# Optimization experiments

Measured on AMD Instinct MI355X. Metric: run time of the kernel, lower is better.

Reference implementation:

```python
import jax, jax.numpy as jnp
import numpy as np

D = 512      # embedding_dimension
L1 = 1024    # english sentence length
L2 = 1024    # french sentence length
V1 = 32000   # english vocab
V2 = 32000   # french vocab
NNEG = 8192  # negative samples
SCALE = 0.05 # param init scale (keeps exp() stable)


def setup_inputs() -> dict:
    key = jax.random.key(0)
    ks = jax.random.split(key, 32)
    def n(k, shape):
        return jax.random.normal(k, shape, dtype=jnp.float32) * SCALE
    inp = {}
    inp["en"] = jax.random.randint(ks[0], (L1,), 0, V1)
    inp["fr"] = jax.random.randint(ks[1], (L2,), 0, V2)
    inp["en_neg"] = jax.random.randint(ks[2], (NNEG,), 0, V1)
    inp["fr_neg"] = jax.random.randint(ks[3], (NNEG,), 0, V2)
    # input embeddings
    inp["emb"] = n(ks[4], (V1, D))
    # 3-layer BiLSTM, hidden=D per direction; layer0 in=D, layers 1-2 in=2D
    inp["Wih0"] = n(ks[5], (2, 4 * D, D)); inp["Whh0"] = n(ks[6], (2, 4 * D, D)); inp["b0"] = n(ks[7], (2, 4 * D))
    inp["Wih1"] = n(ks[8], (2, 4 * D, 2 * D)); inp["Whh1"] = n(ks[9], (2, 4 * D, D)); inp["b1"] = n(ks[10], (2, 4 * D))
    inp["Wih2"] = n(ks[11], (2, 4 * D, 2 * D)); inp["Whh2"] = n(ks[12], (2, 4 * D, D)); inp["b2"] = n(ks[13], (2, 4 * D))
    # inference nets (mu and sigma, 2-layer each)
    inp["Wmu1"] = n(ks[14], (D, D)); inp["bmu1"] = n(ks[15], (D,))
    inp["Wmu2"] = n(ks[16], (D, D)); inp["bmu2"] = n(ks[17], (D,))
    inp["Ws1"] = n(ks[18], (D, D)); inp["bs1"] = n(ks[19], (D,))
    inp["Ws2"] = n(ks[20], (D, D)); inp["bs2"] = n(ks[21], (D,))
    # softmax-approximation embedding tables
    inp["E_en"] = n(ks[22], (V1, D))
    inp["E_fr"] = n(ks[23], (V2, D))
    # reparameterization noise (epsilon.sample() per token, made explicit)
    inp["eps"] = jax.random.normal(ks[24], (L1, D), dtype=jnp.float32)
    return inp


def _lstm_bidir(xs, Wih, Whh, b):
    # xs: (L, in); Wih: (2, 4D, in); Whh: (2, 4D, D); b: (2, 4D)
    def run(d, reverse):
        Wi, Wh, bb = Wih[d], Whh[d], b[d]
        def step(carry, x):
            h, c = carry
            g = Wi @ x + Wh @ h + bb
            i, f, gg, o = jnp.split(g, 4)
            i = jax.nn.sigmoid(i); f = jax.nn.sigmoid(f)
            gg = jnp.tanh(gg); o = jax.nn.sigmoid(o)
            c = f * c + i * gg
            h = o * jnp.tanh(c)
            return (h, c), h
        init = (jnp.zeros((Wh.shape[1],), xs.dtype), jnp.zeros((Wh.shape[1],), xs.dtype))
        _, hs = jax.lax.scan(step, init, xs, reverse=reverse)
        return hs
    return run(0, False), run(1, True)  # each (L, D)


def reference(en, fr, en_neg, fr_neg, emb,
              Wih0, Whh0, b0, Wih1, Whh1, b1, Wih2, Whh2, b2,
              Wmu1, bmu1, Wmu2, bmu2, Ws1, bs1, Ws2, bs2,
              E_en, E_fr, eps):
    x = emb[en]                                   # (L1, D)
    hf, hb = _lstm_bidir(x, Wih0, Whh0, b0)
    hf, hb = _lstm_bidir(jnp.concatenate([hf, hb], -1), Wih1, Whh1, b1)
    hf, hb = _lstm_bidir(jnp.concatenate([hf, hb], -1), Wih2, Whh2, b2)
    h = hf + hb                                   # fwd+bwd hidden sum (intermediate[0][0]+intermediate[0][1])
    mu = jax.nn.relu(h @ Wmu1.T + bmu1) @ Wmu2.T + bmu2
    sigma = jax.nn.softplus(jax.nn.relu(h @ Ws1.T + bs1) @ Ws2.T + bs2)
    z = mu + eps * sigma                          # reparameterized sample (L1, D)
    # closed-form KL( N(mu, diag(sigma^2)) || N(0, I) ), summed over tokens
    kl = 0.5 * jnp.sum(sigma ** 2 + mu ** 2 - 1.0 - 2.0 * jnp.log(sigma))
    # english negative-sampling softmax approximation, summed over tokens
    pos = jnp.exp(jnp.sum(z * E_en[en], axis=-1))            # (L1,)
    neg = jnp.sum(jnp.exp(z @ E_en[en_neg].T), axis=-1)      # (L1,)
    sum_x = jnp.sum(pos / (pos + neg))
    # alignment scoring: every french token vs every english latent z
    s = jnp.exp(z @ E_fr[fr].T)                               # (L1, L2)
    negf = jnp.sum(jnp.exp(z @ E_fr[fr_neg].T), -1, keepdims=True)  # (L1, 1)
    p = s / (s + negf)                                        # (L1, L2)
    sum_y = jnp.sum(p) / L1                                   # uniform-alignment marginal
    return -(sum_x + sum_y - kl)


if __name__ == "__main__":
    out = reference(**setup_inputs())
    print(out)
```

## Files before the change

### kernel.cpp

```cpp
#include <hip/hip_runtime.h>
#include <hip/hip_bf16.h>


template<bool GATHER, bool RELU, int EPI>
__global__ __launch_bounds__(256) void gemm_nt(
    const float* __restrict__ A, const float* __restrict__ B,
    const float* __restrict__ bias, const int* __restrict__ idx,
    float* __restrict__ C, const float* __restrict__ negf,
    float* __restrict__ outsum, int M, int N, int K)
{
    __shared__ float As[16][68];
    __shared__ float Bs[16][68];
    __shared__ float wsum[4];

    const int tid = threadIdx.x;
    const int bm = blockIdx.x, bn = blockIdx.y;
    const int tx = tid & 15, ty = tid >> 4;
    const int lr = tid >> 2;
    const int lk = (tid & 3) * 4;

    const long arow = (long)bm * 64 + lr;
    const int  brow = bn * 64 + lr;
    const long bsrc = GATHER ? (long)idx[brow] : (long)brow;
    const float* Ap = A + arow * K + lk;
    const float* Bp = B + bsrc * K + lk;

    float acc[4][4] = {};

    for (int k0 = 0; k0 < K; k0 += 16) {
        float4 av = *(const float4*)(Ap + k0);
        float4 bv = *(const float4*)(Bp + k0);
        __syncthreads();
        As[lk + 0][lr] = av.x; As[lk + 1][lr] = av.y;
        As[lk + 2][lr] = av.z; As[lk + 3][lr] = av.w;
        Bs[lk + 0][lr] = bv.x; Bs[lk + 1][lr] = bv.y;
        Bs[lk + 2][lr] = bv.z; Bs[lk + 3][lr] = bv.w;
        __syncthreads();
#pragma unroll
        for (int k = 0; k < 16; ++k) {
            float4 a = *(const float4*)&As[k][ty * 4];
            float4 b = *(const float4*)&Bs[k][tx * 4];
            float ar[4] = {a.x, a.y, a.z, a.w};
            float br[4] = {b.x, b.y, b.z, b.w};
#pragma unroll
            for (int i = 0; i < 4; ++i)
#pragma unroll
                for (int j = 0; j < 4; ++j)
                    acc[i][j] += ar[i] * br[j];
        }
    }

    const int row0 = bm * 64 + ty * 4, col0 = bn * 64 + tx * 4;

    if (EPI == 0) {
#pragma unroll
        for (int i = 0; i < 4; ++i) {
            float4 v;
            float vv[4];
#pragma unroll
            for (int j = 0; j < 4; ++j) {
                float x = acc[i][j];
                if (bias) x += bias[col0 + j];
                if (RELU) x = x > 0.f ? x : 0.f;
                vv[j] = x;
            }
            v.x = vv[0]; v.y = vv[1]; v.z = vv[2]; v.w = vv[3];
            *(float4*)&C[(long)(row0 + i) * N + col0] = v;
        }
    } else if (EPI == 1) {
#pragma unroll
        for (int i = 0; i < 4; ++i) {
            float s = expf(acc[i][0]) + expf(acc[i][1]) +
                      expf(acc[i][2]) + expf(acc[i][3]);
            s += __shfl_xor(s, 1); s += __shfl_xor(s, 2);
            s += __shfl_xor(s, 4); s += __shfl_xor(s, 8);
            if (tx == 0) atomicAdd(&C[row0 + i], s);
        }
    } else {
        float t = 0.f;
#pragma unroll
        for (int i = 0; i < 4; ++i) {
            float nf = negf[row0 + i];
#pragma unroll
            for (int j = 0; j < 4; ++j) {
                float e = expf(acc[i][j]);
                t += e / (e + nf);
            }
        }
#pragma unroll
        for (int o = 1; o < 64; o <<= 1) t += __shfl_xor(t, o);
        if ((tid & 63) == 0) wsum[tid >> 6] = t;
        __syncthreads();
        if (tid == 0) atomicAdd(outsum, wsum[0] + wsum[1] + wsum[2] + wsum[3]);
    }
}

__global__ __launch_bounds__(256, 1) void lstm_scan(
    const float* __restrict__ Xf, const float* __restrict__ Xb,
    const float* __restrict__ Whh,
    float* __restrict__ out,
    unsigned long long* __restrict__ hbuf)
{
    const int tid  = threadIdx.x;
    const int dir  = blockIdx.x >> 7;
    const int w    = blockIdx.x & 127;
    const int r    = tid >> 4;
    const int ck   = tid & 15;
    const int gate = r >> 2;
    const int jl   = r & 3;
    const int j    = w * 4 + jl;
    const int grow = gate * 512 + j;

    __shared__ float Wl[256 * 36];
    __shared__ float hs[16 * 36];
    __shared__ float ga[16];

    {
        const float4* Wrow = (const float4*)(Whh + ((long)dir * 2048 + grow) * 512 + ck * 32);
        float4* wl4 = (float4*)Wl + tid * 9;
#pragma unroll
        for (int q = 0; q < 8; ++q) wl4[q] = Wrow[q];
    }
    __syncthreads();

    const float* Xp = dir ? Xb : Xf;
    unsigned long long* myh = hbuf + dir * 1024;

    float c = 0.f;
    bool dead = false;

    const float4* wl4 = (const float4*)Wl + tid * 9;
    const float4* hs4 = (const float4*)hs + ck * 9;

    for (int s = 0; s < 1024; ++s) {
        const int t = dir ? (1023 - s) : s;
        float xg = Xp[(long)t * 2048 + grow];

        unsigned long long* rb = myh + ((s + 1) & 1) * 512;
        unsigned long long v0, v1;
        unsigned it = 0;
        for (;;) {
            v0 = __hip_atomic_load(&rb[tid],       __ATOMIC_RELAXED, __HIP_MEMORY_SCOPE_AGENT);
            v1 = __hip_atomic_load(&rb[tid + 256], __ATOMIC_RELAXED, __HIP_MEMORY_SCOPE_AGENT);
            if (dead || ((int)(v0 >> 32) == s && (int)(v1 >> 32) == s)) break;
            if (++it > (1u << 20)) { dead = true; break; }
        }
        hs[((tid) >> 5) * 36 + (tid & 31)]             = __uint_as_float((unsigned)v0);
        hs[((tid + 256) >> 5) * 36 + (tid & 31)]       = __uint_as_float((unsigned)v1);
        __syncthreads();

        float a0 = 0.f, a1 = 0.f;
#pragma unroll
        for (int q = 0; q < 8; q += 2) {
            float4 w0 = wl4[q],     h0 = hs4[q];
            float4 w1 = wl4[q + 1], h1 = hs4[q + 1];
            a0 += w0.x*h0.x + w0.y*h0.y + w0.z*h0.z + w0.w*h0.w;
            a1 += w1.x*h1.x + w1.y*h1.y + w1.z*h1.z + w1.w*h1.w;
        }
        float acc = a0 + a1;
        acc += __shfl_xor(acc, 1);
        acc += __shfl_xor(acc, 2);
        acc += __shfl_xor(acc, 4);
        acc += __shfl_xor(acc, 8);
        if (ck == 0) ga[r] = acc + xg;
        __syncthreads();

        if (tid < 4) {
            float gi = ga[tid], gf = ga[4 + tid], gg = ga[8 + tid], go = ga[12 + tid];
            float i_ = 1.f / (1.f + __expf(-gi));
            float f_ = 1.f / (1.f + __expf(-gf));
            float eg = __expf(2.f * gg);
            float g_ = (eg - 1.f) / (eg + 1.f);
            float o_ = 1.f / (1.f + __expf(-go));
            c = f_ * c + i_ * g_;
            float ec = __expf(2.f * c);
            float tc = (ec - 1.f) / (ec + 1.f);
            float h = o_ * tc;
            unsigned long long pk = (unsigned long long)__float_as_uint(h)
                                  | ((unsigned long long)(unsigned)(s + 1) << 32);
            __hip_atomic_store(&myh[(s & 1) * 512 + w * 4 + tid], pk,
                               __ATOMIC_RELAXED, __HIP_MEMORY_SCOPE_AGENT);
            out[(long)t * 1024 + dir * 512 + w * 4 + tid] = h;
        }
    }
}

__global__ __launch_bounds__(128) void gather_emb(
    const int* __restrict__ en, const float* __restrict__ emb, float* __restrict__ x0)
{
    const int t = blockIdx.x;
    ((float4*)(x0 + (long)t * 512))[threadIdx.x] =
        ((const float4*)(emb + (long)en[t] * 512))[threadIdx.x];
}

__global__ __launch_bounds__(256) void add_h(
    const float* __restrict__ o2, float* __restrict__ h)
{
    const long i = (long)blockIdx.x * 256 + threadIdx.x;
    const long t = i >> 9, j = i & 511;
    h[i] = o2[t * 1024 + j] + o2[t * 1024 + 512 + j];
}

__global__ __launch_bounds__(256) void zkl_kernel(
    const float* __restrict__ mu, const float* __restrict__ sp,
    const float* __restrict__ eps, float* __restrict__ z, float* __restrict__ klsum)
{
    __shared__ float w4[4];
    const int i = blockIdx.x * 256 + threadIdx.x;
    float m = mu[i], x = sp[i];
    float sg = (x > 20.f) ? x : log1pf(expf(x));
    z[i] = m + eps[i] * sg;
    float kl = 0.5f * (sg * sg + m * m - 1.f) - logf(sg);
#pragma unroll
    for (int o = 1; o < 64; o <<= 1) kl += __shfl_xor(kl, o);
    if ((threadIdx.x & 63) == 0) w4[threadIdx.x >> 6] = kl;
    __syncthreads();
    if (threadIdx.x == 0) atomicAdd(klsum, w4[0] + w4[1] + w4[2] + w4[3]);
}

__global__ __launch_bounds__(64) void pos_kernel(
    const float* __restrict__ z, const float* __restrict__ E_en,
    const int* __restrict__ en, float* __restrict__ pos)
{
    const int t = blockIdx.x, lane = threadIdx.x;
    const float4* zr = (const float4*)(z + (long)t * 512);
    const float4* er = (const float4*)(E_en + (long)en[t] * 512);
    float s = 0.f;
#pragma unroll
    for (int q = 0; q < 2; ++q) {
        float4 a = zr[lane + q * 64], b = er[lane + q * 64];
        s += a.x * b.x + a.y * b.y + a.z * b.z + a.w * b.w;
    }
#pragma unroll
    for (int o = 1; o < 64; o <<= 1) s += __shfl_xor(s, o);
    if (lane == 0) pos[t] = expf(s);
}

__global__ __launch_bounds__(256) void finalize_kernel(
    const float* __restrict__ pos, const float* __restrict__ neg,
    const float* __restrict__ scal, float* __restrict__ out)
{
    __shared__ float w4[4];
    const int tid = threadIdx.x;
    float s = 0.f;
#pragma unroll
    for (int q = 0; q < 4; ++q) {
        int t = tid + q * 256;
        s += pos[t] / (pos[t] + neg[t]);
    }
#pragma unroll
    for (int o = 1; o < 64; o <<= 1) s += __shfl_xor(s, o);
    if ((tid & 63) == 0) w4[tid >> 6] = s;
    __syncthreads();
    if (tid == 0) {
        float sum_x = w4[0] + w4[1] + w4[2] + w4[3];
        out[0] = scal[0] - sum_x - scal[1] * (1.f / 1024.f);
    }
}

extern "C" void kernel_launch(void* const* d_in, const int* in_sizes, int n_in,
                              void* d_out, int out_size, void* d_ws, size_t ws_size,
                              hipStream_t stream)
{
    const int*   en     = (const int*)d_in[0];
    const int*   fr     = (const int*)d_in[1];
    const int*   en_neg = (const int*)d_in[2];
    const int*   fr_neg = (const int*)d_in[3];
    const float* emb    = (const float*)d_in[4];
    const float* Wih0   = (const float*)d_in[5];
    const float* Whh0   = (const float*)d_in[6];
    const float* b0     = (const float*)d_in[7];
    const float* Wih1   = (const float*)d_in[8];
    const float* Whh1   = (const float*)d_in[9];
    const float* b1     = (const float*)d_in[10];
    const float* Wih2   = (const float*)d_in[11];
    const float* Whh2   = (const float*)d_in[12];
    const float* b2     = (const float*)d_in[13];
    const float* Wmu1   = (const float*)d_in[14];
    const float* bmu1   = (const float*)d_in[15];
    const float* Wmu2   = (const float*)d_in[16];
    const float* bmu2   = (const float*)d_in[17];
    const float* Ws1    = (const float*)d_in[18];
    const float* bs1    = (const float*)d_in[19];
    const float* Ws2    = (const float*)d_in[20];
    const float* bs2    = (const float*)d_in[21];
    const float* E_en   = (const float*)d_in[22];
    const float* E_fr   = (const float*)d_in[23];
    const float* eps    = (const float*)d_in[24];
    float* out = (float*)d_out;

    float* w = (float*)d_ws;
    float* x0   = w;  w += 1024 * 512;
    float* bufA = w;  w += 1024 * 1024;
    float* bufB = w;  w += 1024 * 1024;
    float* Xf   = w;  w += 1024 * 2048;
    float* Xb   = w;  w += 1024 * 2048;
    float* h    = w;  w += 1024 * 512;
    float* tmp  = w;  w += 1024 * 512;
    float* mu   = w;  w += 1024 * 512;
    float* sp   = w;  w += 1024 * 512;
    float* z    = w;  w += 1024 * 512;
    float* pos  = w;  w += 1024;
    float* neg  = w;  w += 1024;
    float* negf = w;  w += 1024;
    unsigned long long* hbuf = (unsigned long long*)w; w += 4096;
    float* scal = w;  w += 2;

    hipMemsetAsync(neg, 0, 2048 * sizeof(float), stream);
    hipMemsetAsync(scal, 0, 2 * sizeof(float), stream);

    gather_emb<<<1024, 128, 0, stream>>>(en, emb, x0);

    gemm_nt<false, false, 0><<<dim3(16, 32), 256, 0, stream>>>(
        x0, Wih0,               b0,        nullptr, Xf, nullptr, nullptr, 1024, 2048, 512);
    gemm_nt<false, false, 0><<<dim3(16, 32), 256, 0, stream>>>(
        x0, Wih0 + 2048 * 512,  b0 + 2048, nullptr, Xb, nullptr, nullptr, 1024, 2048, 512);
    hipMemsetAsync(hbuf, 0, 4096 * 8, stream);
    lstm_scan<<<256, 256, 0, stream>>>(Xf, Xb, Whh0, bufA, hbuf);

    gemm_nt<false, false, 0><<<dim3(16, 32), 256, 0, stream>>>(
        bufA, Wih1,               b1,        nullptr, Xf, nullptr, nullptr, 1024, 2048, 1024);
    gemm_nt<false, false, 0><<<dim3(16, 32), 256, 0, stream>>>(
        bufA, Wih1 + 2048 * 1024, b1 + 2048, nullptr, Xb, nullptr, nullptr, 1024, 2048, 1024);
    hipMemsetAsync(hbuf, 0, 4096 * 8, stream);
    lstm_scan<<<256, 256, 0, stream>>>(Xf, Xb, Whh1, bufB, hbuf);

    gemm_nt<false, false, 0><<<dim3(16, 32), 256, 0, stream>>>(
        bufB, Wih2,               b2,        nullptr, Xf, nullptr, nullptr, 1024, 2048, 1024);
    gemm_nt<false, false, 0><<<dim3(16, 32), 256, 0, stream>>>(
        bufB, Wih2 + 2048 * 1024, b2 + 2048, nullptr, Xb, nullptr, nullptr, 1024, 2048, 1024);
    hipMemsetAsync(hbuf, 0, 4096 * 8, stream);
    lstm_scan<<<256, 256, 0, stream>>>(Xf, Xb, Whh2, bufA, hbuf);

    add_h<<<2048, 256, 0, stream>>>(bufA, h);

    gemm_nt<false, true, 0><<<dim3(16, 8), 256, 0, stream>>>(
        h,   Wmu1, bmu1, nullptr, tmp, nullptr, nullptr, 1024, 512, 512);
    gemm_nt<false, false, 0><<<dim3(16, 8), 256, 0, stream>>>(
        tmp, Wmu2, bmu2, nullptr, mu,  nullptr, nullptr, 1024, 512, 512);
    gemm_nt<false, true, 0><<<dim3(16, 8), 256, 0, stream>>>(
        h,   Ws1,  bs1,  nullptr, tmp, nullptr, nullptr, 1024, 512, 512);
    gemm_nt<false, false, 0><<<dim3(16, 8), 256, 0, stream>>>(
        tmp, Ws2,  bs2,  nullptr, sp,  nullptr, nullptr, 1024, 512, 512);

    zkl_kernel<<<2048, 256, 0, stream>>>(mu, sp, eps, z, scal);

    pos_kernel<<<1024, 64, 0, stream>>>(z, E_en, en, pos);
    gemm_nt<true, false, 1><<<dim3(16, 128), 256, 0, stream>>>(
        z, E_en, nullptr, en_neg, neg,  nullptr, nullptr, 1024, 8192, 512);
    gemm_nt<true, false, 1><<<dim3(16, 128), 256, 0, stream>>>(
        z, E_fr, nullptr, fr_neg, negf, nullptr, nullptr, 1024, 8192, 512);
    gemm_nt<true, false, 2><<<dim3(16, 16), 256, 0, stream>>>(
        z, E_fr, nullptr, fr,     nullptr, negf, scal + 1, 1024, 1024, 512);

    finalize_kernel<<<1, 256, 0, stream>>>(pos, neg, scal, out);
}
```

Before: 7.148 ms.

## Restructure LSTM scan so each wavefront owns one hidden unit, dropping a barrier

```diff
diff --git a/kernel.cpp b/kernel.cpp
--- a/kernel.cpp
+++ b/kernel.cpp
@@ -104,16 +104,15 @@
     const int tid  = threadIdx.x;
     const int dir  = blockIdx.x >> 7;
     const int w    = blockIdx.x & 127;
-    const int r    = tid >> 4;
-    const int ck   = tid & 15;
-    const int gate = r >> 2;
-    const int jl   = r & 3;
-    const int j    = w * 4 + jl;
+    const int v    = tid >> 6;
+    const int ln   = tid & 63;
+    const int gate = ln >> 4;
+    const int ck   = ln & 15;
+    const int j    = w * 4 + v;
     const int grow = gate * 512 + j;
 
     __shared__ float Wl[256 * 36];
-    __shared__ float hs[16 * 36];
-    __shared__ float ga[16];
+    __shared__ float hsbuf[2][16 * 36];
 
     {
         const float4* Wrow = (const float4*)(Whh + ((long)dir * 2048 + grow) * 512 + ck * 32);
@@ -128,27 +127,37 @@
 
     float c = 0.f;
     bool dead = false;
-
     const float4* wl4 = (const float4*)Wl + tid * 9;
-    const float4* hs4 = (const float4*)hs + ck * 9;
 
     for (int s = 0; s < 1024; ++s) {
         const int t = dir ? (1023 - s) : s;
         float xg = Xp[(long)t * 2048 + grow];
 
-        unsigned long long* rb = myh + ((s + 1) & 1) * 512;
-        unsigned long long v0, v1;
-        unsigned it = 0;
-        for (;;) {
-            v0 = __hip_atomic_load(&rb[tid],       __ATOMIC_RELAXED, __HIP_MEMORY_SCOPE_AGENT);
-            v1 = __hip_atomic_load(&rb[tid + 256], __ATOMIC_RELAXED, __HIP_MEMORY_SCOPE_AGENT);
-            if (dead || ((int)(v0 >> 32) == s && (int)(v1 >> 32) == s)) break;
-            if (++it > (1u << 20)) { dead = true; break; }
-        }
-        hs[((tid) >> 5) * 36 + (tid & 31)]             = __uint_as_float((unsigned)v0);
-        hs[((tid + 256) >> 5) * 36 + (tid & 31)]       = __uint_as_float((unsigned)v1);
+        float* hs = hsbuf[s & 1];
+
+        if (v == 0) {
+            unsigned long long* rb = myh + ((s + 1) & 1) * 512;
+            unsigned long long vv[8];
+            unsigned it = 0;
+            for (;;) {
+                bool ok = true;
+#pragma unroll
+                for (int k = 0; k < 8; ++k)
+                    vv[k] = __hip_atomic_load(&rb[ln * 8 + k], __ATOMIC_RELAXED,
+                                              __HIP_MEMORY_SCOPE_AGENT);
+#pragma unroll
+                for (int k = 0; k < 8; ++k)
+                    ok &= ((int)(vv[k] >> 32) == s);
+                if (ok || dead) break;
+                if (++it > (1u << 20)) { dead = true; break; }
+            }
+            float* hb = hs + (ln >> 2) * 36 + (ln & 3) * 8;
+#pragma unroll
+            for (int k = 0; k < 8; ++k) hb[k] = __uint_as_float((unsigned)vv[k]);
+        }
         __syncthreads();
 
+        const float4* hs4 = (const float4*)hs + ck * 9;
         float a0 = 0.f, a1 = 0.f;
 #pragma unroll
         for (int q = 0; q < 8; q += 2) {
@@ -157,30 +166,32 @@
             a0 += w0.x*h0.x + w0.y*h0.y + w0.z*h0.z + w0.w*h0.w;
             a1 += w1.x*h1.x + w1.y*h1.y + w1.z*h1.z + w1.w*h1.w;
         }
-        float acc = a0 + a1;
-        acc += __shfl_xor(acc, 1);
-        acc += __shfl_xor(acc, 2);
-        acc += __shfl_xor(acc, 4);
-        acc += __shfl_xor(acc, 8);
-        if (ck == 0) ga[r] = acc + xg;
-        __syncthreads();
-
-        if (tid < 4) {
-            float gi = ga[tid], gf = ga[4 + tid], gg = ga[8 + tid], go = ga[12 + tid];
-            float i_ = 1.f / (1.f + __expf(-gi));
-            float f_ = 1.f / (1.f + __expf(-gf));
-            float eg = __expf(2.f * gg);
-            float g_ = (eg - 1.f) / (eg + 1.f);
-            float o_ = 1.f / (1.f + __expf(-go));
+        float a = a0 + a1;
+        if (ck == 0) a += xg;
+        a += __shfl_xor(a, 1);
+        a += __shfl_xor(a, 2);
+        a += __shfl_xor(a, 4);
+        a += __shfl_xor(a, 8);
+
+        float sgm = 1.f / (1.f + __expf(-a));
+        float e2  = __expf(2.f * a);
+        float th  = (e2 - 1.f) / (e2 + 1.f);
+        float gv  = (gate == 2) ? th : sgm;
+
+        float i_ = gv;
+        float f_ = __shfl(gv, 16);
+        float g_ = __shfl(gv, 32);
+        float o_ = __shfl(gv, 48);
+
+        if (ln == 0) {
             c = f_ * c + i_ * g_;
-            float ec = __expf(2.f * c);
-            float tc = (ec - 1.f) / (ec + 1.f);
-            float h = o_ * tc;
+            float e2c = __expf(2.f * c);
+            float h = o_ * ((e2c - 1.f) / (e2c + 1.f));
             unsigned long long pk = (unsigned long long)__float_as_uint(h)
                                   | ((unsigned long long)(unsigned)(s + 1) << 32);
-            __hip_atomic_store(&myh[(s & 1) * 512 + w * 4 + tid], pk,
+            __hip_atomic_store(&myh[(s & 1) * 512 + j], pk,
                                __ATOMIC_RELAXED, __HIP_MEMORY_SCOPE_AGENT);
-            out[(long)t * 1024 + dir * 512 + w * 4 + tid] = h;
+            out[(long)t * 1024 + dir * 512 + j] = h;
         }
     }
 }
```

New measurement: 11.13 ms. 1.56x slower.

## Run both LSTM directions in each workgroup, halving the scan grid

Applied to the files above, without the earlier changes.

```diff
diff --git a/kernel.cpp b/kernel.cpp
--- a/kernel.cpp
+++ b/kernel.cpp
@@ -102,8 +102,7 @@
     unsigned long long* __restrict__ hbuf)
 {
     const int tid  = threadIdx.x;
-    const int dir  = blockIdx.x >> 7;
-    const int w    = blockIdx.x & 127;
+    const int w    = blockIdx.x;
     const int r    = tid >> 4;
     const int ck   = tid & 15;
     const int gate = r >> 2;
@@ -111,76 +110,135 @@
     const int j    = w * 4 + jl;
     const int grow = gate * 512 + j;
 
-    __shared__ float Wl[256 * 36];
-    __shared__ float hs[16 * 36];
-    __shared__ float ga[16];
+    __shared__ float WlA[256 * 36];
+    __shared__ float WlB[256 * 36];
+    __shared__ float hsA[16 * 36];
+    __shared__ float hsB[16 * 36];
+    __shared__ float gaA[16];
+    __shared__ float gaB[16];
 
     {
-        const float4* Wrow = (const float4*)(Whh + ((long)dir * 2048 + grow) * 512 + ck * 32);
-        float4* wl4 = (float4*)Wl + tid * 9;
-#pragma unroll
-        for (int q = 0; q < 8; ++q) wl4[q] = Wrow[q];
+        const float4* WrowA = (const float4*)(Whh + (long)grow * 512 + ck * 32);
+        const float4* WrowB = (const float4*)(Whh + (long)(2048 + grow) * 512 + ck * 32);
+        float4* wla = (float4*)WlA + tid * 9;
+        float4* wlb = (float4*)WlB + tid * 9;
+#pragma unroll
+        for (int q = 0; q < 8; ++q) { wla[q] = WrowA[q]; wlb[q] = WrowB[q]; }
     }
     __syncthreads();
 
-    const float* Xp = dir ? Xb : Xf;
-    unsigned long long* myh = hbuf + dir * 1024;
-
-    float c = 0.f;
-    bool dead = false;
-
-    const float4* wl4 = (const float4*)Wl + tid * 9;
-    const float4* hs4 = (const float4*)hs + ck * 9;
+    unsigned long long* hb0 = hbuf;
+    unsigned long long* hb1 = hbuf + 1024;
+
+    const float4* wla4 = (const float4*)WlA + tid * 9;
+    const float4* wlb4 = (const float4*)WlB + tid * 9;
+    const float4* hsa4 = (const float4*)hsA + ck * 9;
+    const float4* hsb4 = (const float4*)hsB + ck * 9;
+
+    float cA = 0.f, cB = 0.f;
+    bool deadA = false, deadB = false;
 
     for (int s = 0; s < 1024; ++s) {
-        const int t = dir ? (1023 - s) : s;
-        float xg = Xp[(long)t * 2048 + grow];
-
-        unsigned long long* rb = myh + ((s + 1) & 1) * 512;
-        unsigned long long v0, v1;
-        unsigned it = 0;
-        for (;;) {
-            v0 = __hip_atomic_load(&rb[tid],       __ATOMIC_RELAXED, __HIP_MEMORY_SCOPE_AGENT);
-            v1 = __hip_atomic_load(&rb[tid + 256], __ATOMIC_RELAXED, __HIP_MEMORY_SCOPE_AGENT);
-            if (dead || ((int)(v0 >> 32) == s && (int)(v1 >> 32) == s)) break;
-            if (++it > (1u << 20)) { dead = true; break; }
-        }
-        hs[((tid) >> 5) * 36 + (tid & 31)]             = __uint_as_float((unsigned)v0);
-        hs[((tid + 256) >> 5) * 36 + (tid & 31)]       = __uint_as_float((unsigned)v1);
-        __syncthreads();
-
-        float a0 = 0.f, a1 = 0.f;
-#pragma unroll
-        for (int q = 0; q < 8; q += 2) {
-            float4 w0 = wl4[q],     h0 = hs4[q];
-            float4 w1 = wl4[q + 1], h1 = hs4[q + 1];
-            a0 += w0.x*h0.x + w0.y*h0.y + w0.z*h0.z + w0.w*h0.w;
-            a1 += w1.x*h1.x + w1.y*h1.y + w1.z*h1.z + w1.w*h1.w;
-        }
-        float acc = a0 + a1;
-        acc += __shfl_xor(acc, 1);
-        acc += __shfl_xor(acc, 2);
-        acc += __shfl_xor(acc, 4);
-        acc += __shfl_xor(acc, 8);
-        if (ck == 0) ga[r] = acc + xg;
-        __syncthreads();
-
-        if (tid < 4) {
-            float gi = ga[tid], gf = ga[4 + tid], gg = ga[8 + tid], go = ga[12 + tid];
-            float i_ = 1.f / (1.f + __expf(-gi));
-            float f_ = 1.f / (1.f + __expf(-gf));
-            float eg = __expf(2.f * gg);
-            float g_ = (eg - 1.f) / (eg + 1.f);
-            float o_ = 1.f / (1.f + __expf(-go));
-            c = f_ * c + i_ * g_;
-            float ec = __expf(2.f * c);
-            float tc = (ec - 1.f) / (ec + 1.f);
-            float h = o_ * tc;
-            unsigned long long pk = (unsigned long long)__float_as_uint(h)
-                                  | ((unsigned long long)(unsigned)(s + 1) << 32);
-            __hip_atomic_store(&myh[(s & 1) * 512 + w * 4 + tid], pk,
-                               __ATOMIC_RELAXED, __HIP_MEMORY_SCOPE_AGENT);
-            out[(long)t * 1024 + dir * 512 + w * 4 + tid] = h;
+        const int tA = s, tB = 1023 - s;
+        float xgA = Xf[(long)tA * 2048 + grow];
+        float xgB = Xb[(long)tB * 2048 + grow];
+
+        {
+            unsigned long long* rb = hb0 + ((s + 1) & 1) * 512;
+            unsigned long long v0, v1;
+            unsigned it = 0;
+            for (;;) {
+                v0 = __hip_atomic_load(&rb[tid],       __ATOMIC_RELAXED, __HIP_MEMORY_SCOPE_AGENT);
+                v1 = __hip_atomic_load(&rb[tid + 256], __ATOMIC_RELAXED, __HIP_MEMORY_SCOPE_AGENT);
+                if (deadA || ((int)(v0 >> 32) == s && (int)(v1 >> 32) == s)) break;
+                __builtin_amdgcn_s_sleep(1);
+                if (++it > (1u << 20)) { deadA = true; break; }
+            }
+            hsA[(tid >> 5) * 36 + (tid & 31)]         = __uint_as_float((unsigned)v0);
+            hsA[((tid + 256) >> 5) * 36 + (tid & 31)] = __uint_as_float((unsigned)v1);
+            __syncthreads();
+
+            float a0 = 0.f, a1 = 0.f;
+#pragma unroll
+            for (int q = 0; q < 8; q += 2) {
+                float4 w0 = wla4[q],     h0 = hsa4[q];
+                float4 w1 = wla4[q + 1], h1 = hsa4[q + 1];
+                a0 += w0.x*h0.x + w0.y*h0.y + w0.z*h0.z + w0.w*h0.w;
+                a1 += w1.x*h1.x + w1.y*h1.y + w1.z*h1.z + w1.w*h1.w;
+            }
+            float acc = a0 + a1;
+            acc += __shfl_xor(acc, 1);
+            acc += __shfl_xor(acc, 2);
+            acc += __shfl_xor(acc, 4);
+            acc += __shfl_xor(acc, 8);
+            if (ck == 0) gaA[r] = acc + xgA;
+            __syncthreads();
+
+            if (tid < 4) {
+                float gi = gaA[tid], gf = gaA[4 + tid], gg = gaA[8 + tid], go = gaA[12 + tid];
+                float i_ = 1.f / (1.f + __expf(-gi));
+                float f_ = 1.f / (1.f + __expf(-gf));
+                float eg = __expf(2.f * gg);
+                float g_ = (eg - 1.f) / (eg + 1.f);
+                float o_ = 1.f / (1.f + __expf(-go));
+                cA = f_ * cA + i_ * g_;
+                float ec = __expf(2.f * cA);
+                float h = o_ * ((ec - 1.f) / (ec + 1.f));
+                unsigned long long pk = (unsigned long long)__float_as_uint(h)
+                                      | ((unsigned long long)(unsigned)(s + 1) << 32);
+                __hip_atomic_store(&hb0[(s & 1) * 512 + w * 4 + tid], pk,
+                                   __ATOMIC_RELAXED, __HIP_MEMORY_SCOPE_AGENT);
+                out[(long)tA * 1024 + w * 4 + tid] = h;
+            }
+        }
+
+        {
+            unsigned long long* rb = hb1 + ((s + 1) & 1) * 512;
+            unsigned long long v0, v1;
+            unsigned it = 0;
+            for (;;) {
+                v0 = __hip_atomic_load(&rb[tid],       __ATOMIC_RELAXED, __HIP_MEMORY_SCOPE_AGENT);
+                v1 = __hip_atomic_load(&rb[tid + 256], __ATOMIC_RELAXED, __HIP_MEMORY_SCOPE_AGENT);
+                if (deadB || ((int)(v0 >> 32) == s && (int)(v1 >> 32) == s)) break;
+                __builtin_amdgcn_s_sleep(1);
+                if (++it > (1u << 20)) { deadB = true; break; }
+            }
+            hsB[(tid >> 5) * 36 + (tid & 31)]         = __uint_as_float((unsigned)v0);
+            hsB[((tid + 256) >> 5) * 36 + (tid & 31)] = __uint_as_float((unsigned)v1);
+            __syncthreads();
+
+            float a0 = 0.f, a1 = 0.f;
+#pragma unroll
+            for (int q = 0; q < 8; q += 2) {
+                float4 w0 = wlb4[q],     h0 = hsb4[q];
+                float4 w1 = wlb4[q + 1], h1 = hsb4[q + 1];
+                a0 += w0.x*h0.x + w0.y*h0.y + w0.z*h0.z + w0.w*h0.w;
+                a1 += w1.x*h1.x + w1.y*h1.y + w1.z*h1.z + w1.w*h1.w;
+            }
+            float acc = a0 + a1;
+            acc += __shfl_xor(acc, 1);
+            acc += __shfl_xor(acc, 2);
+            acc += __shfl_xor(acc, 4);
+            acc += __shfl_xor(acc, 8);
+            if (ck == 0) gaB[r] = acc + xgB;
+            __syncthreads();
+
+            if (tid < 4) {
+                float gi = gaB[tid], gf = gaB[4 + tid], gg = gaB[8 + tid], go = gaB[12 + tid];
+                float i_ = 1.f / (1.f + __expf(-gi));
+                float f_ = 1.f / (1.f + __expf(-gf));
+                float eg = __expf(2.f * gg);
+                float g_ = (eg - 1.f) / (eg + 1.f);
+                float o_ = 1.f / (1.f + __expf(-go));
+                cB = f_ * cB + i_ * g_;
+                float ec = __expf(2.f * cB);
+                float h = o_ * ((ec - 1.f) / (ec + 1.f));
+                unsigned long long pk = (unsigned long long)__float_as_uint(h)
+                                      | ((unsigned long long)(unsigned)(s + 1) << 32);
+                __hip_atomic_store(&hb1[(s & 1) * 512 + w * 4 + tid], pk,
+                                   __ATOMIC_RELAXED, __HIP_MEMORY_SCOPE_AGENT);
+                out[(long)tB * 1024 + 512 + w * 4 + tid] = h;
+            }
         }
     }
 }
@@ -316,21 +374,21 @@
     gemm_nt<false, false, 0><<<dim3(16, 32), 256, 0, stream>>>(
         x0, Wih0 + 2048 * 512,  b0 + 2048, nullptr, Xb, nullptr, nullptr, 1024, 2048, 512);
     hipMemsetAsync(hbuf, 0, 4096 * 8, stream);
-    lstm_scan<<<256, 256, 0, stream>>>(Xf, Xb, Whh0, bufA, hbuf);
+    lstm_scan<<<128, 256, 0, stream>>>(Xf, Xb, Whh0, bufA, hbuf);
 
     gemm_nt<false, false, 0><<<dim3(16, 32), 256, 0, stream>>>(
         bufA, Wih1,               b1,        nullptr, Xf, nullptr, nullptr, 1024, 2048, 1024);
     gemm_nt<false, false, 0><<<dim3(16, 32), 256, 0, stream>>>(
         bufA, Wih1 + 2048 * 1024, b1 + 2048, nullptr, Xb, nullptr, nullptr, 1024, 2048, 1024);
     hipMemsetAsync(hbuf, 0, 4096 * 8, stream);
-    lstm_scan<<<256, 256, 0, stream>>>(Xf, Xb, Whh1, bufB, hbuf);
+    lstm_scan<<<128, 256, 0, stream>>>(Xf, Xb, Whh1, bufB, hbuf);
 
     gemm_nt<false, false, 0><<<dim3(16, 32), 256, 0, stream>>>(
         bufB, Wih2,               b2,        nullptr, Xf, nullptr, nullptr, 1024, 2048, 1024);
     gemm_nt<false, false, 0><<<dim3(16, 32), 256, 0, stream>>>(
         bufB, Wih2 + 2048 * 1024, b2 + 2048, nullptr, Xb, nullptr, nullptr, 1024, 2048, 1024);
     hipMemsetAsync(hbuf, 0, 4096 * 8, stream);
-    lstm_scan<<<256, 256, 0, stream>>>(Xf, Xb, Whh2, bufA, hbuf);
+    lstm_scan<<<128, 256, 0, stream>>>(Xf, Xb, Whh2, bufA, hbuf);
 
     add_h<<<2048, 256, 0, stream>>>(bufA, h);
 
```

After: 7.950 ms. 1.11x slower.
